# Performance work log

Hardware: AMD Instinct MI355X
Metric: run time of the kernel (lower is better)

Reference implementation:

```python
import jax, jax.numpy as jnp
import numpy as np

B, H, W = 1, 1024, 2048
NX = 2048
H_STEP = 6.0 / NX            # h = length_x / nx
COF = 1.0                    # TEMPER_COEFFICIENT
DIFF = 0.0                   # self.diff_coeff
WC0V = 651.83 * 202.412 * 0.001 / 2.0   # wc0 = WC0*TH0*0.001/THcell
C1, C2, C4, N_EXP, CT = 0.65248278, 0.002, 400.0, 0.5, 1.0
FLUX0 = 300.0                # self.flux value used inside evp()

# 3x3 'valid' stencils on the reflect-padded field (match torch conv2d cross-correlation)
def _dx(x):
    return 0.5 * (x[..., 1:-1, 2:] - x[..., 1:-1, :-2])

def _dy(x):
    return 0.5 * (x[..., 2:, 1:-1] - x[..., :-2, 1:-1])

def _lap(x):
    return (x[..., 1:-1, 2:] + x[..., 1:-1, :-2] + x[..., 2:, 1:-1]
            + x[..., :-2, 1:-1] - 4.0 * x[..., 1:-1, 1:-1])

def _evp(tmp, wc_bc):
    t = tmp + 273.15
    cp_a = (28.11 + 1.967e-3 * t + 4.802e-6 * t**2 - 1.966e-9 * t**3) / 28.97 * 1000.0
    cp_v = (32.24 + 1.923e-3 * t + 10.55e-6 * t**2 - 3.595e-9 * t**3) / 18.015 * 1000.0
    P_v = jnp.exp(23.2 - 3816.4 / (t - 46.1))
    x_v = 0.62198 * P_v / (101325.0 - P_v)
    x_a = 0.00725
    C3 = jnp.power(jnp.mean(wc_bc) / WC0V, N_EXP)
    porous = C1 * C2 * C3 * C4 * CT
    m_dot = FLUX0 / (cp_a + cp_v * x_a) * (x_v - x_a) * porous
    return m_dot


def _forward(layout, heat_ini, wc, heat, flow):
    u = flow[..., 0, :, :]                      # [B,H,W]
    v = flow[..., 1, :, :]
    b = layout[:, 1].squeeze()                  # [H,W] int boundary codes
    geom = layout[:, 0].astype(heat.dtype)      # [B,H,W]
    geom = geom.at[..., 0, :].set(1.0).at[..., -1, :].set(1.0)
    # in-place boundary edits, same order as torch
    b = (b.at[1, 1:].set(0).at[-2, 1:].set(0).at[:, 1].set(0)
          .at[:, -1].set(3).at[0, :].set(3).at[-1, :].set(3))

    wc_mask = (b > 3).astype(wc.dtype)          # [H,W], broadcasts like torch [1,1,H,W]
    wc_bc = wc * wc_mask
    bc_mask = (b != 1).astype(heat.dtype)       # set_bc(1, tmp=0): mask 0, value 0
    heat_bc = heat * bc_mask

    xp = jnp.pad(heat_bc, ((0, 0), (0, 0), (1, 1), (1, 1)), mode='reflect')
    m_dot = _evp(heat_bc, wc_bc)                # evp called twice with identical state
    src = 300.0 * H_STEP                        # self.src (evp_src returns 0)
    flux = 300.0 * H_STEP                       # self.flux at apply_Energy time

    dx_, dy_ = _dx(xp), _dy(xp)                 # [B,1,H,W]
    ad = heat_ini - 0.001 * (u * dx_ + v * dy_ - DIFF * _lap(xp) / H_STEP)
    wcv = WC0V - 0.001 * m_dot                  # self.wc(wc)

    extras = {0: 0.0, 2: 0.0, 3: 0.0,
              4: flux * dx_ + wcv, 5: -flux * dy_ + wcv,
              6: -flux * dx_ + wcv, 7: flux * dy_ + wcv,
              8: flux * (-dx_ + dy_) + wcv, 9: flux * (dy_ + dx_) + wcv,
              10: flux * (dx_ - dy_) + wcv, 11: flux * (-dx_ - dy_) + wcv}
    loss_eq = jnp.zeros_like(heat)
    eq_mask = jnp.zeros_like(b)
    for eq in [0, 2, 3, 4, 5, 6, 7, 8, 9, 10, 11]:   # fixed small set, not a data dim
        m = (b == eq)
        eq_mask = jnp.where(m, eq, eq_mask)
        loss_eq = loss_eq + m.astype(heat.dtype) * (ad + extras[eq])

    f = COF * jnp.abs(geom - 1.0) * src * H_STEP     # [B,H,W]
    energy_loss = jnp.mean((loss_eq - f[:, None]) ** 2)
    wc_loss = jnp.mean((WC0V * wc_mask - m_dot - wc_bc) ** 2)
    return energy_loss + wc_loss, heat_bc, eq_mask


def setup_inputs() -> dict:
    key = jax.random.key(0)
    k1, k2, k3, k4, k5 = jax.random.split(key, 5)
    layout = jax.random.randint(k1, (B, 2, H, W), 0, 12, dtype=jnp.int32)
    heat_ini = jax.random.normal(k2, (B, 1, H, W), dtype=jnp.float32)
    wc = jax.random.uniform(k3, (B, 1, H, W), dtype=jnp.float32)
    heat = jax.random.normal(k4, (B, 1, H, W), dtype=jnp.float32)
    flow = jax.random.normal(k5, (B, 2, H, W), dtype=jnp.float32)
    return {"layout": layout, "heat_ini": heat_ini, "wc": wc, "heat": heat, "flow": flow}


def reference(layout, heat_ini, wc, heat, flow):
    return _forward(layout, heat_ini, wc, heat, flow)
```

## Files before the change

### kernel.cpp

```cpp
#include <hip/hip_runtime.h>
#include <math.h>

#define H_ 1024
#define W_ 2048
#define HW_ (H_ * W_)
#define NB_ 1024

#define FLUXF     0.87890625f
#define F_FACT    0.002574920654296875f
#define WC0VF     65.96910698f
#define POROUS_K  0.521986224f

__device__ __forceinline__ int fix_b(int raw, int i, int j) {
    if (i == 0 || i == H_ - 1) return 3;
    if (j == W_ - 1) return 3;
    if (j == 1) return 0;
    if ((i == 1 || i == H_ - 2) && j >= 1) return 0;
    return raw;
}

__global__ __launch_bounds__(256)
void k_main(const int* __restrict__ layout, const float* __restrict__ heat_ini,
            const float* __restrict__ wc, const float* __restrict__ heat,
            const float* __restrict__ flow, float* __restrict__ out_hb,
            float* __restrict__ out_eq, float* __restrict__ ws) {
    const int i  = blockIdx.x;
    const int jb = threadIdx.x << 3;
    const int im = (i == 0) ? 1 : i - 1;
    const int ip = (i == H_ - 1) ? H_ - 2 : i + 1;
    const int* L1 = layout + HW_;
    const int base  = i * W_ + jb;
    const int baseu = im * W_ + jb;
    const int based = ip * W_ + jb;

    int4   bc0 = *(const int4*)(L1 + base),      bc1 = *(const int4*)(L1 + base + 4);
    int4   bu0 = *(const int4*)(L1 + baseu),     bu1 = *(const int4*)(L1 + baseu + 4);
    int4   bd0 = *(const int4*)(L1 + based),     bd1 = *(const int4*)(L1 + based + 4);
    int4   g0  = *(const int4*)(layout + base),  g1  = *(const int4*)(layout + base + 4);
    float4 hc0 = *(const float4*)(heat + base),  hc1 = *(const float4*)(heat + base + 4);
    float4 hu0 = *(const float4*)(heat + baseu), hu1 = *(const float4*)(heat + baseu + 4);
    float4 hd0 = *(const float4*)(heat + based), hd1 = *(const float4*)(heat + based + 4);
    float4 hi0 = *(const float4*)(heat_ini + base), hi1 = *(const float4*)(heat_ini + base + 4);
    float4 w0  = *(const float4*)(wc + base),    w1  = *(const float4*)(wc + base + 4);
    float4 u0  = *(const float4*)(flow + base),  u1  = *(const float4*)(flow + base + 4);
    float4 v0  = *(const float4*)(flow + HW_ + base), v1 = *(const float4*)(flow + HW_ + base + 4);

    int   bcs[8] = {bc0.x,bc0.y,bc0.z,bc0.w, bc1.x,bc1.y,bc1.z,bc1.w};
    int   bus[8] = {bu0.x,bu0.y,bu0.z,bu0.w, bu1.x,bu1.y,bu1.z,bu1.w};
    int   bds[8] = {bd0.x,bd0.y,bd0.z,bd0.w, bd1.x,bd1.y,bd1.z,bd1.w};
    int   gs[8]  = {g0.x,g0.y,g0.z,g0.w, g1.x,g1.y,g1.z,g1.w};
    float hcs[8] = {hc0.x,hc0.y,hc0.z,hc0.w, hc1.x,hc1.y,hc1.z,hc1.w};
    float hus[8] = {hu0.x,hu0.y,hu0.z,hu0.w, hu1.x,hu1.y,hu1.z,hu1.w};
    float hds[8] = {hd0.x,hd0.y,hd0.z,hd0.w, hd1.x,hd1.y,hd1.z,hd1.w};
    float his[8] = {hi0.x,hi0.y,hi0.z,hi0.w, hi1.x,hi1.y,hi1.z,hi1.w};
    float wss[8] = {w0.x,w0.y,w0.z,w0.w, w1.x,w1.y,w1.z,w1.w};
    float us[8]  = {u0.x,u0.y,u0.z,u0.w, u1.x,u1.y,u1.z,u1.w};
    float vs[8]  = {v0.x,v0.y,v0.z,v0.w, v1.x,v1.y,v1.z,v1.w};

    __shared__ float shb[W_];
    int   bfix[8];
    float hb8[8], oeqs[8];
    #pragma unroll
    for (int k = 0; k < 8; k++) {
        int b = fix_b(bcs[k], i, jb + k);
        bfix[k] = b;
        hb8[k]  = (b != 1) ? hcs[k] : 0.0f;
        oeqs[k] = (b == 1) ? 0.0f : (float)b;
    }
    *(float4*)(shb + jb)     = make_float4(hb8[0], hb8[1], hb8[2], hb8[3]);
    *(float4*)(shb + jb + 4) = make_float4(hb8[4], hb8[5], hb8[6], hb8[7]);
    *(float4*)(out_hb + base)     = make_float4(hb8[0], hb8[1], hb8[2], hb8[3]);
    *(float4*)(out_hb + base + 4) = make_float4(hb8[4], hb8[5], hb8[6], hb8[7]);
    *(float4*)(out_eq + base)     = make_float4(oeqs[0], oeqs[1], oeqs[2], oeqs[3]);
    *(float4*)(out_eq + base + 4) = make_float4(oeqs[4], oeqs[5], oeqs[6], oeqs[7]);
    __syncthreads();

    float acc[7] = {0.f,0.f,0.f,0.f,0.f,0.f,0.f};
    #pragma unroll
    for (int k = 0; k < 8; k++) {
        int j = jb + k;
        int b = bfix[k];
        float hl = (k == 0) ? ((j == 0) ? 0.0f : shb[j - 1]) : hb8[k - 1];
        float hr = (k == 7) ? ((j == W_ - 1) ? 0.0f : shb[j + 1]) : hb8[k + 1];
        float dx = (j == 0 || j == W_ - 1) ? 0.0f : 0.5f * (hr - hl);
        float hbu = (fix_b(bus[k], im, j) != 1) ? hus[k] : 0.0f;
        float hbd = (fix_b(bds[k], ip, j) != 1) ? hds[k] : 0.0f;
        float dy = 0.5f * (hbd - hbu);

        float ad = his[k] - 0.001f * (us[k] * dx + vs[k] * dy);

        float t  = hb8[k] + 273.15f;
        float t2 = t * t, t3 = t2 * t;
        float cp_a = (28.11f + 0.001967f * t + 4.802e-6f * t2 - 1.966e-9f * t3)
                     * (1000.0f / 28.97f);
        float cp_v = (32.24f + 0.001923f * t + 1.055e-5f * t2 - 3.595e-9f * t3)
                     * (1000.0f / 18.015f);
        float P_v = expf(23.2f - 3816.4f / (t - 46.1f));
        float x_v = 0.62198f * P_v / (101325.0f - P_v);
        float q = 300.0f / (cp_a + cp_v * 0.00725f) * (x_v - 0.00725f);

        float f = (i == 0 || i == H_ - 1) ? 0.0f
                  : fabsf((float)gs[k] - 1.0f) * F_FACT;

        float a_e, c_e;
        if (b == 1) {
            a_e = -f; c_e = 0.0f;
        } else {
            float cx = (b == 4 || b == 9 || b == 10) ? 1.0f
                     : ((b == 6 || b == 8 || b == 11) ? -1.0f : 0.0f);
            float cy = (b == 7 || b == 8 || b == 9) ? 1.0f
                     : ((b == 5 || b == 10 || b == 11) ? -1.0f : 0.0f);
            float extra0 = (b >= 4) ? (FLUXF * (cx * dx + cy * dy) + WC0VF) : 0.0f;
            a_e = ad + extra0 - f;
            c_e = (b >= 4) ? (-0.001f * q) : 0.0f;
        }
        acc[1] += a_e * a_e;
        acc[2] += a_e * c_e;
        acc[3] += c_e * c_e;

        float wm  = (b > 3) ? 1.0f : 0.0f;
        float wcb = wm * wss[k];
        float aw  = WC0VF * wm - wcb;
        acc[0] += wcb;
        acc[4] += aw * aw;
        acc[5] += aw * q;
        acc[6] += q * q;
    }

    #pragma unroll
    for (int off = 32; off > 0; off >>= 1) {
        #pragma unroll
        for (int s = 0; s < 7; s++) acc[s] += __shfl_down(acc[s], off, 64);
    }
    __shared__ float red[4][7];
    int lane = threadIdx.x & 63, wid = threadIdx.x >> 6;
    if (lane == 0) {
        #pragma unroll
        for (int s = 0; s < 7; s++) red[wid][s] = acc[s];
    }
    __syncthreads();
    if (threadIdx.x == 0) {
        #pragma unroll
        for (int s = 0; s < 7; s++)
            ws[s * NB_ + blockIdx.x] =
                red[0][s] + red[1][s] + red[2][s] + red[3][s];
    }
}

__global__ __launch_bounds__(256)
void k_final(const float* __restrict__ ws, float* __restrict__ out) {
    __shared__ float sred[7][4];
    int tid = threadIdx.x;
    #pragma unroll
    for (int s = 0; s < 7; s++) {
        float4 x = *(const float4*)(ws + s * NB_ + (tid << 2));
        float a = x.x + x.y + x.z + x.w;
        #pragma unroll
        for (int off = 32; off > 0; off >>= 1) a += __shfl_down(a, off, 64);
        if ((tid & 63) == 0) sred[s][tid >> 6] = a;
    }
    __syncthreads();
    if (tid == 0) {
        float S[7];
        #pragma unroll
        for (int s = 0; s < 7; s++)
            S[s] = sred[s][0] + sred[s][1] + sred[s][2] + sred[s][3];
        float mean_wc = S[0] * (1.0f / (float)HW_);
        float p = POROUS_K * sqrtf(mean_wc / WC0VF);
        float energy = S[1] + 2.0f * p * S[2] + p * p * S[3];
        float wcl    = S[4] - 2.0f * p * S[5] + p * p * S[6];
        out[0] = (energy + wcl) * (1.0f / (float)HW_);
    }
}

extern "C" void kernel_launch(void* const* d_in, const int* in_sizes, int n_in,
                              void* d_out, int out_size, void* d_ws, size_t ws_size,
                              hipStream_t stream) {
    const int*   layout   = (const int*)d_in[0];
    const float* heat_ini = (const float*)d_in[1];
    const float* wc       = (const float*)d_in[2];
    const float* heat     = (const float*)d_in[3];
    const float* flow     = (const float*)d_in[4];
    float* out = (float*)d_out;
    float* ws  = (float*)d_ws;

    float* out_hb = out + 1;
    float* out_eq = out + 1 + HW_;

    k_main<<<NB_, 256, 0, stream>>>(layout, heat_ini, wc, heat, flow,
                                    out_hb, out_eq, ws);
    k_final<<<1, 256, 0, stream>>>(ws, out);
}
```

Baseline: 114.7 us.

## Split each row across two 128-thread blocks with swizzled block order

Each row is now handled by two half-row blocks of 128 threads instead of one 256-thread block, doubling the grid to 2048 blocks. Block indices are remapped so consecutive blocks land on rows spread across the grid, which may change how work is distributed over XCDs and caches. Halo columns at the half-row boundary are loaded by edge threads into a padded shared buffer. The final reduction is widened to sum 2048 partials per statistic. This trades extra halo loads for finer scheduling granularity and better occupancy balance.

```diff
diff --git a/kernel.cpp b/kernel.cpp
--- a/kernel.cpp
+++ b/kernel.cpp
@@ -4,7 +4,9 @@
 #define H_ 1024
 #define W_ 2048
 #define HW_ (H_ * W_)
-#define NB_ 1024
+#define NB_ 2048
+#define TPB_ 128
+#define HALF_ 1024
 
 #define FLUXF     0.87890625f
 #define F_FACT    0.002574920654296875f
@@ -19,13 +21,17 @@
     return raw;
 }
 
-__global__ __launch_bounds__(256)
+__global__ __launch_bounds__(TPB_)
 void k_main(const int* __restrict__ layout, const float* __restrict__ heat_ini,
             const float* __restrict__ wc, const float* __restrict__ heat,
             const float* __restrict__ flow, float* __restrict__ out_hb,
             float* __restrict__ out_eq, float* __restrict__ ws) {
-    const int i  = blockIdx.x;
-    const int jb = threadIdx.x << 3;
+    const int virt = ((blockIdx.x & 7) << 8) | (blockIdx.x >> 3);
+    const int i    = virt >> 1;
+    const int jb0  = (virt & 1) * HALF_;
+    const int tid  = threadIdx.x;
+    const int lj   = tid << 3;
+    const int jb   = jb0 + lj;
     const int im = (i == 0) ? 1 : i - 1;
     const int ip = (i == H_ - 1) ? H_ - 2 : i + 1;
     const int* L1 = layout + HW_;
@@ -45,6 +51,24 @@
     float4 u0  = *(const float4*)(flow + base),  u1  = *(const float4*)(flow + base + 4);
     float4 v0  = *(const float4*)(flow + HW_ + base), v1 = *(const float4*)(flow + HW_ + base + 4);
 
+    __shared__ float shb[HALF_ + 2];
+    if (tid == 0) {
+        float hv = 0.0f;
+        if (jb0 != 0) {
+            int j = jb0 - 1;
+            hv = (fix_b(L1[i * W_ + j], i, j) != 1) ? heat[i * W_ + j] : 0.0f;
+        }
+        shb[0] = hv;
+    }
+    if (tid == TPB_ - 1) {
+        float hv = 0.0f;
+        if (jb0 + HALF_ < W_) {
+            int j = jb0 + HALF_;
+            hv = (fix_b(L1[i * W_ + j], i, j) != 1) ? heat[i * W_ + j] : 0.0f;
+        }
+        shb[HALF_ + 1] = hv;
+    }
+
     int   bcs[8] = {bc0.x,bc0.y,bc0.z,bc0.w, bc1.x,bc1.y,bc1.z,bc1.w};
     int   bus[8] = {bu0.x,bu0.y,bu0.z,bu0.w, bu1.x,bu1.y,bu1.z,bu1.w};
     int   bds[8] = {bd0.x,bd0.y,bd0.z,bd0.w, bd1.x,bd1.y,bd1.z,bd1.w};
@@ -57,7 +81,6 @@
     float us[8]  = {u0.x,u0.y,u0.z,u0.w, u1.x,u1.y,u1.z,u1.w};
     float vs[8]  = {v0.x,v0.y,v0.z,v0.w, v1.x,v1.y,v1.z,v1.w};
 
-    __shared__ float shb[W_];
     int   bfix[8];
     float hb8[8], oeqs[8];
     #pragma unroll
@@ -67,8 +90,8 @@
         hb8[k]  = (b != 1) ? hcs[k] : 0.0f;
         oeqs[k] = (b == 1) ? 0.0f : (float)b;
     }
-    *(float4*)(shb + jb)     = make_float4(hb8[0], hb8[1], hb8[2], hb8[3]);
-    *(float4*)(shb + jb + 4) = make_float4(hb8[4], hb8[5], hb8[6], hb8[7]);
+    *(float4*)(shb + 1 + lj)     = make_float4(hb8[0], hb8[1], hb8[2], hb8[3]);
+    *(float4*)(shb + 1 + lj + 4) = make_float4(hb8[4], hb8[5], hb8[6], hb8[7]);
     *(float4*)(out_hb + base)     = make_float4(hb8[0], hb8[1], hb8[2], hb8[3]);
     *(float4*)(out_hb + base + 4) = make_float4(hb8[4], hb8[5], hb8[6], hb8[7]);
     *(float4*)(out_eq + base)     = make_float4(oeqs[0], oeqs[1], oeqs[2], oeqs[3]);
@@ -80,8 +103,8 @@
     for (int k = 0; k < 8; k++) {
         int j = jb + k;
         int b = bfix[k];
-        float hl = (k == 0) ? ((j == 0) ? 0.0f : shb[j - 1]) : hb8[k - 1];
-        float hr = (k == 7) ? ((j == W_ - 1) ? 0.0f : shb[j + 1]) : hb8[k + 1];
+        float hl = (k == 0) ? shb[lj]     : hb8[k - 1];
+        float hr = (k == 7) ? shb[lj + 9] : hb8[k + 1];
         float dx = (j == 0 || j == W_ - 1) ? 0.0f : 0.5f * (hr - hl);
         float hbu = (fix_b(bus[k], im, j) != 1) ? hus[k] : 0.0f;
         float hbd = (fix_b(bds[k], ip, j) != 1) ? hds[k] : 0.0f;
@@ -132,7 +155,7 @@
         #pragma unroll
         for (int s = 0; s < 7; s++) acc[s] += __shfl_down(acc[s], off, 64);
     }
-    __shared__ float red[4][7];
+    __shared__ float red[2][7];
     int lane = threadIdx.x & 63, wid = threadIdx.x >> 6;
     if (lane == 0) {
         #pragma unroll
@@ -142,8 +165,7 @@
     if (threadIdx.x == 0) {
         #pragma unroll
         for (int s = 0; s < 7; s++)
-            ws[s * NB_ + blockIdx.x] =
-                red[0][s] + red[1][s] + red[2][s] + red[3][s];
+            ws[s * NB_ + blockIdx.x] = red[0][s] + red[1][s];
     }
 }
 
@@ -153,8 +175,9 @@
     int tid = threadIdx.x;
     #pragma unroll
     for (int s = 0; s < 7; s++) {
-        float4 x = *(const float4*)(ws + s * NB_ + (tid << 2));
-        float a = x.x + x.y + x.z + x.w;
+        float4 x = *(const float4*)(ws + s * NB_ + (tid << 3));
+        float4 y = *(const float4*)(ws + s * NB_ + (tid << 3) + 4);
+        float a = (x.x + x.y + x.z + x.w) + (y.x + y.y + y.z + y.w);
         #pragma unroll
         for (int off = 32; off > 0; off >>= 1) a += __shfl_down(a, off, 64);
         if ((tid & 63) == 0) sred[s][tid >> 6] = a;
@@ -187,7 +210,7 @@
     float* out_hb = out + 1;
     float* out_eq = out + 1 + HW_;
 
-    k_main<<<NB_, 256, 0, stream>>>(layout, heat_ini, wc, heat, flow,
-                                    out_hb, out_eq, ws);
+    k_main<<<NB_, TPB_, 0, stream>>>(layout, heat_ini, wc, heat, flow,
+                                     out_hb, out_eq, ws);
     k_final<<<1, 256, 0, stream>>>(ws, out);
 }
```

Measured after the change: 111.4 us. -2.9%, faster.
